# Performance work log

Measured on AMD Instinct MI355X. Metric: run time of the kernel, lower is better.

Reference implementation:

```python
import jax, jax.numpy as jnp
import numpy as np

B, S, E = 2, 2048, 5120
HQ, HKV, HD = 32, 8, 128          # q heads, kv heads, head_dim (hard-coded 128 in source)
DQ, DKV = HQ * HD, HKV * HD       # 4096, 1024
ROPE_THETA = 1.0e9
NEG = -1e30


def setup_inputs() -> dict:
    key = jax.random.key(0)
    k0, k1, k2, k3, k4 = jax.random.split(key, 5)
    x = jax.random.normal(k0, (B, S, E), jnp.float32)
    wq = jax.random.normal(k1, (DQ, E), jnp.float32) * 0.02
    wk = jax.random.normal(k2, (DKV, E), jnp.float32) * 0.02
    wv = jax.random.normal(k3, (DKV, E), jnp.float32) * 0.02
    wo = jax.random.normal(k4, (E, DQ), jnp.float32) * 0.02
    # rotary frequencies: complex freqs_cis[s, HD//2] = exp(i * s * theta^{-2j/HD})
    inv_freq = 1.0 / (ROPE_THETA ** (jnp.arange(0, HD, 2, dtype=jnp.float32) / HD))  # [64]
    ang = jnp.arange(S, dtype=jnp.float32)[:, None] * inv_freq[None, :]              # [S, 64]
    return {
        "x": x,
        "freqs_cos": jnp.cos(ang),
        "freqs_sin": jnp.sin(ang),
        "wq": wq, "wk": wk, "wv": wv, "wo": wo,
    }


def _apply_rope(t, cos, sin):
    # t: [b, s, h, HD//2, 2] viewed as complex pairs; cos/sin: [1, s, 1, HD//2]
    tr, ti = t[..., 0], t[..., 1]
    out = jnp.stack([tr * cos - ti * sin, tr * sin + ti * cos], axis=-1)
    b, s, h = t.shape[0], t.shape[1], t.shape[2]
    return out.reshape(b, s, h, HD)


def reference(x, freqs_cos, freqs_sin, wq, wk, wv, wo):
    b, s, _ = x.shape
    q = (x @ wq.T).reshape(b, s, HQ, HD // 2, 2)
    k = (x @ wk.T).reshape(b, s, HKV, HD // 2, 2)
    v = (x @ wv.T).reshape(b, s, HKV, HD)
    cos = freqs_cos[:s][None, :, None, :]
    sin = freqs_sin[:s][None, :, None, :]
    q = _apply_rope(q, cos, sin)                       # [b, s, HQ, HD]
    k = _apply_rope(k, cos, sin)                       # [b, s, HKV, HD]
    # GQA repeat_kv (repeat_interleave along head dim)
    k = jnp.repeat(k, HQ // HKV, axis=2)               # [b, s, HQ, HD]
    v = jnp.repeat(v, HQ // HKV, axis=2)
    q = q.transpose(0, 2, 1, 3)                        # [b, HQ, s, HD]
    k = k.transpose(0, 2, 1, 3)
    v = v.transpose(0, 2, 1, 3)
    scale = 1.0 / np.sqrt(HD).astype(np.float32)
    scores = jnp.einsum('bhqd,bhkd->bhqk', q, k) * scale
    causal = jnp.tril(jnp.ones((s, s), dtype=bool))
    scores = jnp.where(causal[None, None], scores, NEG)
    attn = jax.nn.softmax(scores, axis=-1)
    out = jnp.einsum('bhqk,bhkd->bhqd', attn, v)       # [b, HQ, s, HD]
    out = out.transpose(0, 2, 1, 3).reshape(b, s, DQ)
    return out @ wo.T                                  # [b, s, E]
```

## Files before the change

### kernel.cpp

```cpp
#include <hip/hip_runtime.h>


typedef unsigned short u16;
typedef __bf16 bf16x8 __attribute__((ext_vector_type(8)));
typedef __bf16 bf16x4 __attribute__((ext_vector_type(4)));
typedef float f32x4 __attribute__((ext_vector_type(4)));

__device__ __forceinline__ u16 f2bf(float f) {
  unsigned u = __builtin_bit_cast(unsigned, f);
  u += 0x7fff + ((u >> 16) & 1);
  return (u16)(u >> 16);
}
__device__ __forceinline__ float bf2f(u16 h) {
  unsigned u = ((unsigned)h) << 16;
  return __builtin_bit_cast(float, u);
}

__device__ __forceinline__ float exp2_hw(float x) {
#if __has_builtin(__builtin_amdgcn_exp2f)
  return __builtin_amdgcn_exp2f(x);
#else
  return __expf(x * 0.6931471805599453f);
#endif
}

__device__ __forceinline__ void gload_lds16(const u16* g, u16* lds) {
  __builtin_amdgcn_global_load_lds(
      (const __attribute__((address_space(1))) void*)g,
      (__attribute__((address_space(3))) void*)lds, 16, 0, 0);
}

__device__ __forceinline__ f32x4 mfma16(bf16x8 a, bf16x8 b, f32x4 c) {
  return __builtin_amdgcn_mfma_f32_16x16x32_bf16(a, b, c, 0, 0, 0);
}

#define VMW(N) asm volatile("s_waitcnt vmcnt(" #N ")" ::: "memory")
#define BAR()  __builtin_amdgcn_s_barrier()

__global__ __launch_bounds__(256) void cvt_kernel(const float4* __restrict__ in,
                                                  uint2* __restrict__ out, int n4) {
  int i = blockIdx.x * blockDim.x + threadIdx.x;
  if (i >= n4) return;
  float4 v = in[i];
  unsigned lo = (unsigned)f2bf(v.x) | ((unsigned)f2bf(v.y) << 16);
  unsigned hi = (unsigned)f2bf(v.z) | ((unsigned)f2bf(v.w) << 16);
  out[i] = make_uint2(lo, hi);
}

__global__ __launch_bounds__(256) void rope_kernel(u16* __restrict__ t,
                                                   const float* __restrict__ fcos,
                                                   const float* __restrict__ fsin,
                                                   int hsh, float scale, int total) {
  int idx = blockIdx.x * blockDim.x + threadIdx.x;
  if (idx >= total) return;
  int j = idx & 63;
  int s = (idx >> (6 + hsh)) & 2047;
  float c = fcos[s * 64 + j], sn = fsin[s * 64 + j];
  unsigned* p = (unsigned*)(t + (size_t)idx * 2);
  unsigned v = *p;
  float tr = bf2f((u16)(v & 0xffffu)), ti = bf2f((u16)(v >> 16));
  float orr = (tr * c - ti * sn) * scale;
  float oi  = (tr * sn + ti * c) * scale;
  *p = (unsigned)f2bf(orr) | ((unsigned)f2bf(oi) << 16);
}

template <int MODE>
__global__ __launch_bounds__(256) void gemm_bt(const u16* __restrict__ A,
                                               const u16* __restrict__ B,
                                               void* __restrict__ Cout,
                                               int M, int N, int K) {
  __shared__ u16 As[8192];
  __shared__ u16 Bs[8192];
  const int tid = threadIdx.x;
  const int lane = tid & 63, wave = tid >> 6;
  const int wm = wave >> 1, wn = wave & 1;
  int gx = gridDim.x, nwg = gx * gridDim.y;
  int lin = blockIdx.y * gx + blockIdx.x;
  if ((nwg & 7) == 0) lin = (lin & 7) * (nwg >> 3) + (lin >> 3);
  const int m0 = (lin / gx) * 128, n0 = (lin % gx) * 128;
  const int lc = lane & 15, lg = lane >> 4;

  f32x4 acc[4][4] = {};
  const int sr = tid >> 3, sc = tid & 7;

  for (int kt = 0; kt < K; kt += 64) {
    __syncthreads();
#pragma unroll
    for (int q = 0; q < 4; ++q) {
      int r = q * 32 + sr;
      int cc = sc ^ (r & 7);
      gload_lds16(A + (size_t)(m0 + r) * K + kt + cc * 8, &As[q * 2048 + tid * 8]);
      gload_lds16(B + (size_t)(n0 + r) * K + kt + cc * 8, &Bs[q * 2048 + tid * 8]);
    }
    __syncthreads();
#pragma unroll
    for (int ks = 0; ks < 2; ++ks) {
      bf16x8 af[4], bfr[4];
#pragma unroll
      for (int m = 0; m < 4; ++m) {
        int r = wm * 64 + m * 16 + lc;
        int gc = ks * 4 + lg;
        af[m] = *(const bf16x8*)&As[r * 64 + ((gc ^ (r & 7)) * 8)];
      }
#pragma unroll
      for (int n = 0; n < 4; ++n) {
        int r = wn * 64 + n * 16 + lc;
        int gc = ks * 4 + lg;
        bfr[n] = *(const bf16x8*)&Bs[r * 64 + ((gc ^ (r & 7)) * 8)];
      }
#pragma unroll
      for (int m = 0; m < 4; ++m)
#pragma unroll
        for (int n = 0; n < 4; ++n)
          acc[m][n] = mfma16(af[m], bfr[n], acc[m][n]);
    }
  }

#pragma unroll
  for (int m = 0; m < 4; ++m) {
#pragma unroll
    for (int n = 0; n < 4; ++n) {
#pragma unroll
      for (int i = 0; i < 4; ++i) {
        int gm = m0 + wm * 64 + m * 16 + lg * 4 + i;
        int gn = n0 + wn * 64 + n * 16 + lc;
        float v = acc[m][n][i];
        if (MODE == 0) {
          ((u16*)Cout)[(size_t)gm * N + gn] = f2bf(v);
        } else if (MODE == 2) {
          size_t addr = ((size_t)((gm >> 11) * 8 + (gn >> 7)) * 128 + (gn & 127)) * 2048 +
                        (gm & 2047);
          ((u16*)Cout)[addr] = f2bf(v);
        } else {
          if (gn < 1024) {
            ((u16*)Cout)[(size_t)gm * 1024 + gn] = f2bf(v);
          } else {
            int gnv = gn - 1024;
            size_t addr = 4194304ull +
                          ((size_t)((gm >> 11) * 8 + (gnv >> 7)) * 128 + (gnv & 127)) * 2048 +
                          (gm & 2047);
            ((u16*)Cout)[addr] = f2bf(v);
          }
        }
      }
    }
  }
}

template <int OUT_F32>
__global__ __launch_bounds__(512, 2) void gemm256(const u16* __restrict__ A,
                                                  const u16* __restrict__ B,
                                                  void* __restrict__ Cout,
                                                  int M, int N, int K) {
  __shared__ u16 lds[2][2][2][8192];
  __shared__ u16 dummy[4096];
  const int tid = threadIdx.x, lane = tid & 63, wave = tid >> 6;
  const int wm = wave >> 2;
  const int wn = wave & 3;
  const int lc = lane & 15, lg = lane >> 4;
  const int bh = wn >> 1;
  const int bs64 = (wn & 1) * 64;
  const int str = tid >> 3, ssc = tid & 7;

  int gx = gridDim.x, nwg = gx * gridDim.y;
  int lin = blockIdx.y * gx + blockIdx.x;
  if ((nwg & 7) == 0) lin = (lin & 7) * (nwg >> 3) + (lin >> 3);
  const int m0 = (lin / gx) * 256, n0 = (lin % gx) * 256;

  auto stageA = [&](int buf, int kcol, int r0, bool real) {
    int r = r0 + str, cc = ssc ^ (r & 7);
    const u16* s = A + (size_t)(m0 + r) * K + kcol + cc * 8;
    u16* d0 = real ? &lds[buf][0][0][r0 * 64] : dummy;
    u16* d1 = real ? &lds[buf][0][1][r0 * 64] : dummy;
    gload_lds16(s, d0 + tid * 8);
    gload_lds16(s + (size_t)128 * K, d1 + tid * 8);
  };
  auto stageB = [&](int buf, int kcol, int half, bool real) {
    int r = str, cc = ssc ^ (r & 7);
    int r2 = 64 + str, cc2 = ssc ^ (r2 & 7);
    const u16* s = B + (size_t)(n0 + half * 128) * K + kcol;
    u16* d0 = real ? &lds[buf][1][half][0] : dummy;
    u16* d1 = real ? &lds[buf][1][half][4096] : dummy;
    gload_lds16(s + (size_t)r * K + cc * 8, d0 + tid * 8);
    gload_lds16(s + (size_t)r2 * K + cc2 * 8, d1 + tid * 8);
  };

  f32x4 acc[8][4] = {};
  bf16x8 af[4][2], bfv[4][2];

  const int nk = K >> 6;
  stageB(0, 0, 0, true);
  stageA(0, 0, 0, true);
  stageB(0, 0, 1, true);
  stageA(0, 0, 64, true);
  stageB(1, 64, 0, true);
  stageA(1, 64, 0, true);
  VMW(6);
  BAR();

  for (int t = 0; t < nk; ++t) {
    const int c = t & 1;
    const int t1 = t + 1, t2 = t + 2;
    const int kc1 = (t1 < nk ? t1 : nk - 1) << 6;
    const int kc2 = (t2 < nk ? t2 : nk - 1) << 6;
    const bool h1 = t1 < nk, h2 = t2 < nk;
    const u16* Ab = &lds[c][0][wm][0];
    const u16* Bb = &lds[c][1][bh][0];

#pragma unroll
    for (int m = 0; m < 4; ++m)
#pragma unroll
      for (int kg = 0; kg < 2; ++kg) {
        int r = m * 16 + lc;
        af[m][kg] = *(const bf16x8*)&Ab[r * 64 + (((kg * 4 + lg) ^ (r & 7)) * 8)];
      }
#pragma unroll
    for (int n = 0; n < 2; ++n)
#pragma unroll
      for (int kg = 0; kg < 2; ++kg) {
        int r = bs64 + n * 16 + lc;
        bfv[n][kg] = *(const bf16x8*)&Bb[r * 64 + (((kg * 4 + lg) ^ (r & 7)) * 8)];
      }
    stageB(t1 & 1, kc1, 1, h1);
    BAR();
    __builtin_amdgcn_s_setprio(1);
#pragma unroll
    for (int m = 0; m < 4; ++m)
#pragma unroll
      for (int n = 0; n < 2; ++n)
#pragma unroll
        for (int kg = 0; kg < 2; ++kg)
          acc[m][n] = mfma16(af[m][kg], bfv[n][kg], acc[m][n]);
    __builtin_amdgcn_s_setprio(0);
    BAR();

#pragma unroll
    for (int n = 2; n < 4; ++n)
#pragma unroll
      for (int kg = 0; kg < 2; ++kg) {
        int r = bs64 + n * 16 + lc;
        bfv[n][kg] = *(const bf16x8*)&Bb[r * 64 + (((kg * 4 + lg) ^ (r & 7)) * 8)];
      }
    stageA(t1 & 1, kc1, 64, h1);
    VMW(6);
    BAR();
    __builtin_amdgcn_s_setprio(1);
#pragma unroll
    for (int m = 0; m < 4; ++m)
#pragma unroll
      for (int n = 2; n < 4; ++n)
#pragma unroll
        for (int kg = 0; kg < 2; ++kg)
          acc[m][n] = mfma16(af[m][kg], bfv[n][kg], acc[m][n]);
    __builtin_amdgcn_s_setprio(0);
    BAR();

#pragma unroll
    for (int m = 0; m < 4; ++m)
#pragma unroll
      for (int kg = 0; kg < 2; ++kg) {
        int r = 64 + m * 16 + lc;
        af[m][kg] = *(const bf16x8*)&Ab[r * 64 + (((kg * 4 + lg) ^ (r & 7)) * 8)];
      }
    stageB(t2 & 1, kc2, 0, h2);
    BAR();
    __builtin_amdgcn_s_setprio(1);
#pragma unroll
    for (int m = 0; m < 4; ++m)
#pragma unroll
      for (int n = 0; n < 2; ++n)
#pragma unroll
        for (int kg = 0; kg < 2; ++kg)
          acc[4 + m][n] = mfma16(af[m][kg], bfv[n][kg], acc[4 + m][n]);
    __builtin_amdgcn_s_setprio(0);
    BAR();

    stageA(t2 & 1, kc2, 0, h2);
    VMW(6);
    BAR();
    __builtin_amdgcn_s_setprio(1);
#pragma unroll
    for (int m = 0; m < 4; ++m)
#pragma unroll
      for (int n = 2; n < 4; ++n)
#pragma unroll
        for (int kg = 0; kg < 2; ++kg)
          acc[4 + m][n] = mfma16(af[m][kg], bfv[n][kg], acc[4 + m][n]);
    __builtin_amdgcn_s_setprio(0);
    BAR();
  }

#pragma unroll
  for (int m = 0; m < 8; ++m) {
#pragma unroll
    for (int n = 0; n < 4; ++n) {
#pragma unroll
      for (int i = 0; i < 4; ++i) {
        int gm = m0 + wm * 128 + m * 16 + lg * 4 + i;
        int gn = n0 + wn * 64 + n * 16 + lc;
        float v = acc[m][n][i];
        if (OUT_F32) ((float*)Cout)[(size_t)gm * N + gn] = v;
        else         ((u16*)Cout)[(size_t)gm * N + gn] = f2bf(v);
      }
    }
  }
}

__global__ __launch_bounds__(512) void attn_kernel(const u16* __restrict__ Q,
                                                   const u16* __restrict__ Kg,
                                                   const u16* __restrict__ VT,
                                                   const float* __restrict__ fcos,
                                                   const float* __restrict__ fsin,
                                                   u16* __restrict__ AO) {
  __shared__ u16 Ks[2][8192];
  __shared__ u16 Vs[2][8192];
  __shared__ u16 P_lds[8][16 * 72];
  const int tid = threadIdx.x, lane = tid & 63, w = tid >> 6;
  const int qt = (int)gridDim.x - 1 - (int)blockIdx.x;
  const int h = blockIdx.y, b = blockIdx.z;
  const int hkv = h >> 2;
  const int q0 = qt * 128;
  const int lc = lane & 15, lg = lane >> 4;

  const float qs = 0.12751743558818574f;
  const int srow = q0 + w * 16 + lc;
  bf16x8 qf[4];
  {
    const size_t qrow = ((size_t)(b * 2048 + srow) * 32 + h) * 128;
#pragma unroll
    for (int ks = 0; ks < 4; ++ks) {
      bf16x8 raw = *(const bf16x8*)&Q[qrow + ks * 32 + lg * 8];
      float4 c4 = *(const float4*)&fcos[srow * 64 + ks * 16 + lg * 4];
      float4 s4 = *(const float4*)&fsin[srow * 64 + ks * 16 + lg * 4];
#pragma unroll
      for (int p = 0; p < 4; ++p) {
        float cc = (&c4.x)[p], ss = (&s4.x)[p];
        float tr = (float)raw[2 * p], ti = (float)raw[2 * p + 1];
        qf[ks][2 * p]     = (__bf16)((tr * cc - ti * ss) * qs);
        qf[ks][2 * p + 1] = (__bf16)((tr * ss + ti * cc) * qs);
      }
    }
  }

  f32x4 o[8] = {};
  f32x4 lsum = {0.f, 0.f, 0.f, 0.f};

  const int nsteps = 2 * qt + 2;
  const size_t kpanel = ((size_t)b * 2048 * 8 + hkv) * 128;
  const size_t vpanel = ((size_t)(b * 8 + hkv) * 128) * 2048;

  auto stage = [&](int buf, int step) {
    const int kv0 = step * 64;
#pragma unroll
    for (int p = 0; p < 2; ++p) {
      int r = p * 32 + (tid >> 4);
      int cc = (tid & 15) ^ (r & 15);
      gload_lds16(Kg + kpanel + (size_t)(kv0 + r) * 1024 + cc * 8,
                  &Ks[buf][p * 4096 + tid * 8]);
    }
#pragma unroll
    for (int p = 0; p < 2; ++p) {
      int r = p * 64 + (tid >> 3);
      int cc = (tid & 7) ^ (r & 7);
      gload_lds16(VT + vpanel + (size_t)r * 2048 + kv0 + cc * 8,
                  &Vs[buf][p * 4096 + tid * 8]);
    }
  };

  stage(0, 0);

  for (int step = 0; step < nsteps; ++step) {
    const int kv0 = step * 64;
    __syncthreads();
    if (step + 1 < nsteps) stage((step + 1) & 1, step + 1);
    const u16* kb = Ks[step & 1];
    const u16* vb = Vs[step & 1];

    f32x4 s[4];
#pragma unroll
    for (int nf = 0; nf < 4; ++nf) s[nf] = f32x4{0.f, 0.f, 0.f, 0.f};
    __builtin_amdgcn_s_setprio(1);
#pragma unroll
    for (int ks = 0; ks < 4; ++ks) {
#pragma unroll
      for (int nf = 0; nf < 4; ++nf) {
        int r = nf * 16 + lc;
        int gc = ks * 4 + lg;
        bf16x8 kf = *(const bf16x8*)&kb[r * 128 + ((gc ^ (r & 15)) * 8)];
        s[nf] = mfma16(kf, qf[ks], s[nf]);
      }
    }
    __builtin_amdgcn_s_setprio(0);

    if (step >= 2 * qt) {
      int q = srow;
#pragma unroll
      for (int nf = 0; nf < 4; ++nf) {
#pragma unroll
        for (int i = 0; i < 4; ++i) {
          int kv = kv0 + nf * 16 + lg * 4 + i;
          if (kv > q) s[nf][i] = -1e30f;
        }
      }
    }

#pragma unroll
    for (int nf = 0; nf < 4; ++nf) {
#pragma unroll
      for (int i = 0; i < 4; ++i) s[nf][i] = exp2_hw(s[nf][i]);
      lsum += s[nf];
      bf16x4 pw = {(__bf16)s[nf][0], (__bf16)s[nf][1], (__bf16)s[nf][2], (__bf16)s[nf][3]};
      *(bf16x4*)&P_lds[w][lc * 72 + nf * 16 + lg * 4] = pw;
    }
    asm volatile("s_waitcnt lgkmcnt(0)" ::: "memory");
    __builtin_amdgcn_sched_barrier(0);

    bf16x8 pa[2];
#pragma unroll
    for (int ksv = 0; ksv < 2; ++ksv)
      pa[ksv] = *(const bf16x8*)&P_lds[w][lc * 72 + ksv * 32 + lg * 8];

    __builtin_amdgcn_s_setprio(1);
#pragma unroll
    for (int nfd = 0; nfd < 8; ++nfd) {
#pragma unroll
      for (int ksv = 0; ksv < 2; ++ksv) {
        int r = nfd * 16 + lc;
        int gc = ksv * 4 + lg;
        bf16x8 vf = *(const bf16x8*)&vb[r * 64 + ((gc ^ (r & 7)) * 8)];
        o[nfd] = mfma16(pa[ksv], vf, o[nfd]);
      }
    }
    __builtin_amdgcn_s_setprio(0);
  }

  float t = lsum[0] + lsum[1] + lsum[2] + lsum[3];
  t += __shfl_xor(t, 16, 64);
  t += __shfl_xor(t, 32, 64);
  float linv[4];
#pragma unroll
  for (int i = 0; i < 4; ++i) linv[i] = 1.0f / __shfl(t, lg * 4 + i, 64);

#pragma unroll
  for (int nfd = 0; nfd < 8; ++nfd)
#pragma unroll
    for (int i = 0; i < 4; ++i) {
      int row = q0 + w * 16 + lg * 4 + i;
      AO[((size_t)(b * 2048 + row) * 32 + h) * 128 + nfd * 16 + lc] =
          f2bf(o[nfd][i] * linv[i]);
    }
}

extern "C" void kernel_launch(void* const* d_in, const int* in_sizes, int n_in,
                              void* d_out, int out_size, void* d_ws, size_t ws_size,
                              hipStream_t stream) {
  const float* x    = (const float*)d_in[0];
  const float* fcos = (const float*)d_in[1];
  const float* fsin = (const float*)d_in[2];
  const float* wq   = (const float*)d_in[3];
  const float* wk   = (const float*)d_in[4];
  const float* wv   = (const float*)d_in[5];
  const float* wo   = (const float*)d_in[6];
  float* out = (float*)d_out;

  char* ws = (char*)d_ws;
  u16* xb  = (u16*)(ws + 0);
  u16* wqb = (u16*)(ws + 41943040ull);
  u16* wkb = (u16*)(ws + 83886080ull);
  u16* wvb = (u16*)(ws + 94371840ull);
  u16* Qb  = (u16*)(ws + 104857600ull);
  u16* Kb  = (u16*)(ws + 138412032ull);
  u16* VTb = (u16*)(ws + 146800640ull);
  u16* AOb = xb;
  u16* wob = wqb;

  auto cvt = [&](const float* src, u16* dst, int nelem) {
    int n4 = nelem / 4;
    cvt_kernel<<<dim3((n4 + 255) / 256), dim3(256), 0, stream>>>((const float4*)src,
                                                                 (uint2*)dst, n4);
  };
  cvt(x, xb, 2 * 2048 * 5120);
  cvt(wq, wqb, 4096 * 5120);
  cvt(wk, wkb, 1024 * 5120);
  cvt(wv, wvb, 1024 * 5120);

  dim3 blk(256);
  gemm256<0><<<dim3(16, 16), dim3(512), 0, stream>>>(xb, wqb, Qb, 4096, 4096, 5120);
  gemm_bt<3><<<dim3(16, 32), blk, 0, stream>>>(xb, wkb, Kb, 4096, 2048, 5120);

  cvt(wo, wob, 5120 * 4096);

  rope_kernel<<<dim3(2097152 / 256), blk, 0, stream>>>(Kb, fcos, fsin, 3, 1.0f, 2097152);

  attn_kernel<<<dim3(16, 32, 2), dim3(512), 0, stream>>>(Qb, Kb, VTb, fcos, fsin, AOb);

  gemm256<1><<<dim3(20, 16), dim3(512), 0, stream>>>(AOb, wob, out, 4096, 5120, 4096);
}
```

Before: 749.1 us.

## Software-pipeline attention loop: overlap next-step QK with current softmax and PV

Restructures the attention main loop into a two-stage software pipeline: the QK^T MFMAs for step t+1 are issued before the softmax and PV work for step t. K staging is split from V staging so K can be loaded two steps ahead. K is triple-buffered in LDS to make room for this, and the loop is unrolled by two with alternating score registers. The aim is to hide exp and LDS latency behind matrix work. The cost is more LDS use, more live registers and an extra barrier per step.

```diff
diff --git a/kernel.cpp b/kernel.cpp
--- a/kernel.cpp
+++ b/kernel.cpp
@@ -312,7 +312,7 @@
                                                    const float* __restrict__ fcos,
                                                    const float* __restrict__ fsin,
                                                    u16* __restrict__ AO) {
-  __shared__ u16 Ks[2][8192];
+  __shared__ u16 Ks[3][8192];
   __shared__ u16 Vs[2][8192];
   __shared__ u16 P_lds[8][16 * 72];
   const int tid = threadIdx.x, lane = tid & 63, w = tid >> 6;
@@ -349,7 +349,7 @@
   const size_t kpanel = ((size_t)b * 2048 * 8 + hkv) * 128;
   const size_t vpanel = ((size_t)(b * 8 + hkv) * 128) * 2048;
 
-  auto stage = [&](int buf, int step) {
+  auto stageK = [&](int buf, int step) {
     const int kv0 = step * 64;
 #pragma unroll
     for (int p = 0; p < 2; ++p) {
@@ -358,6 +358,9 @@
       gload_lds16(Kg + kpanel + (size_t)(kv0 + r) * 1024 + cc * 8,
                   &Ks[buf][p * 4096 + tid * 8]);
     }
+  };
+  auto stageV = [&](int buf, int step) {
+    const int kv0 = step * 64;
 #pragma unroll
     for (int p = 0; p < 2; ++p) {
       int r = p * 64 + (tid >> 3);
@@ -367,16 +370,8 @@
     }
   };
 
-  stage(0, 0);
-
-  for (int step = 0; step < nsteps; ++step) {
-    const int kv0 = step * 64;
-    __syncthreads();
-    if (step + 1 < nsteps) stage((step + 1) & 1, step + 1);
-    const u16* kb = Ks[step & 1];
-    const u16* vb = Vs[step & 1];
-
-    f32x4 s[4];
+  auto qk = [&](f32x4* s, int step) {
+    const u16* kb = Ks[step % 3];
 #pragma unroll
     for (int nf = 0; nf < 4; ++nf) s[nf] = f32x4{0.f, 0.f, 0.f, 0.f};
     __builtin_amdgcn_s_setprio(1);
@@ -391,19 +386,18 @@
       }
     }
     __builtin_amdgcn_s_setprio(0);
-
+  };
+
+  auto softpv = [&](f32x4* s, int step) {
     if (step >= 2 * qt) {
-      int q = srow;
-#pragma unroll
-      for (int nf = 0; nf < 4; ++nf) {
+#pragma unroll
+      for (int nf = 0; nf < 4; ++nf)
 #pragma unroll
         for (int i = 0; i < 4; ++i) {
-          int kv = kv0 + nf * 16 + lg * 4 + i;
-          if (kv > q) s[nf][i] = -1e30f;
+          int kv = step * 64 + nf * 16 + lg * 4 + i;
+          if (kv > srow) s[nf][i] = -1e30f;
         }
-      }
-    }
-
+    }
 #pragma unroll
     for (int nf = 0; nf < 4; ++nf) {
 #pragma unroll
@@ -414,12 +408,11 @@
     }
     asm volatile("s_waitcnt lgkmcnt(0)" ::: "memory");
     __builtin_amdgcn_sched_barrier(0);
-
     bf16x8 pa[2];
 #pragma unroll
     for (int ksv = 0; ksv < 2; ++ksv)
       pa[ksv] = *(const bf16x8*)&P_lds[w][lc * 72 + ksv * 32 + lg * 8];
-
+    const u16* vb = Vs[step & 1];
     __builtin_amdgcn_s_setprio(1);
 #pragma unroll
     for (int nfd = 0; nfd < 8; ++nfd) {
@@ -432,6 +425,25 @@
       }
     }
     __builtin_amdgcn_s_setprio(0);
+  };
+
+  f32x4 sA[4], sB[4];
+  stageK(0, 0); stageV(0, 0);
+  __syncthreads();
+  stageK(1, 1);
+  qk(sA, 0);
+
+  for (int t = 0; t < nsteps; t += 2) {
+    __syncthreads();
+    if (t + 2 < nsteps) stageK((t + 2) % 3, t + 2);
+    if (t + 1 < nsteps) stageV((t + 1) & 1, t + 1);
+    if (t + 1 < nsteps) qk(sB, t + 1);
+    softpv(sA, t);
+    __syncthreads();
+    if (t + 3 < nsteps) stageK((t + 3) % 3, t + 3);
+    if (t + 2 < nsteps) stageV((t + 2) & 1, t + 2);
+    if (t + 2 < nsteps) qk(sA, t + 2);
+    softpv(sB, t + 1);
   }
 
   float t = lsum[0] + lsum[1] + lsum[2] + lsum[3];
```

Result: no change. 756.5 us (+1.0%).

## Remap GEMM workgroups to XCD-local 2D tile blocks and fuse input conversions

Applied to the files above, without the earlier changes.

Replaces the linear XCD-interleave workgroup remap in both GEMM kernels with a 2D decomposition. Each of the 8 XCDs now owns a contiguous rectangular block of output tiles, so A and B panels are reused within that XCD's L2. Also merges the four separate fp32-to-bf16 conversion launches into one grid-stride kernel to cut launch overhead. The remap falls back to a plain row-major order when grid dimensions do not divide evenly. The fused converter adds per-element branching to select the source array.

```diff
diff --git a/kernel.cpp b/kernel.cpp
--- a/kernel.cpp
+++ b/kernel.cpp
@@ -36,6 +36,29 @@
 
 #define VMW(N) asm volatile("s_waitcnt vmcnt(" #N ")" ::: "memory")
 #define BAR()  __builtin_amdgcn_s_barrier()
+
+__global__ __launch_bounds__(256) void cvt4_kernel(const float4* __restrict__ s0,
+                                                   const float4* __restrict__ s1,
+                                                   const float4* __restrict__ s2,
+                                                   const float4* __restrict__ s3,
+                                                   uint2* __restrict__ d0,
+                                                   uint2* __restrict__ d1,
+                                                   uint2* __restrict__ d2,
+                                                   uint2* __restrict__ d3,
+                                                   int n0, int n1, int n2, int n3) {
+  int total = n0 + n1 + n2 + n3;
+  for (int i = blockIdx.x * blockDim.x + threadIdx.x; i < total;
+       i += gridDim.x * blockDim.x) {
+    const float4* s; uint2* d; int j = i;
+    if (j < n0) { s = s0; d = d0; }
+    else if ((j -= n0) < n1) { s = s1; d = d1; }
+    else if ((j -= n1) < n2) { s = s2; d = d2; }
+    else { j -= n2; s = s3; d = d3; }
+    float4 v = s[j];
+    d[j] = make_uint2((unsigned)f2bf(v.x) | ((unsigned)f2bf(v.y) << 16),
+                      (unsigned)f2bf(v.z) | ((unsigned)f2bf(v.w) << 16));
+  }
+}
 
 __global__ __launch_bounds__(256) void cvt_kernel(const float4* __restrict__ in,
                                                   uint2* __restrict__ out, int n4) {
@@ -74,10 +97,18 @@
   const int tid = threadIdx.x;
   const int lane = tid & 63, wave = tid >> 6;
   const int wm = wave >> 1, wn = wave & 1;
-  int gx = gridDim.x, nwg = gx * gridDim.y;
-  int lin = blockIdx.y * gx + blockIdx.x;
-  if ((nwg & 7) == 0) lin = (lin & 7) * (nwg >> 3) + (lin >> 3);
-  const int m0 = (lin / gx) * 128, n0 = (lin % gx) * 128;
+  int gx = gridDim.x, gy = gridDim.y, nwg = gx * gy;
+  int orig = blockIdx.y * gx + blockIdx.x;
+  int mb, nb;
+  if ((gx & 1) == 0 && (gy & 3) == 0 && (nwg & 7) == 0) {
+    int x = orig & 7, idx = orig >> 3;
+    int hy = gy >> 2, qx = gx >> 1;
+    mb = (x >> 1) * hy + (idx % hy);
+    nb = (x & 1) * qx + (idx / hy);
+  } else {
+    mb = orig / gx; nb = orig % gx;
+  }
+  const int m0 = mb * 128, n0 = nb * 128;
   const int lc = lane & 15, lg = lane >> 4;
 
   f32x4 acc[4][4] = {};
@@ -162,10 +193,18 @@
   const int bs64 = (wn & 1) * 64;
   const int str = tid >> 3, ssc = tid & 7;
 
-  int gx = gridDim.x, nwg = gx * gridDim.y;
-  int lin = blockIdx.y * gx + blockIdx.x;
-  if ((nwg & 7) == 0) lin = (lin & 7) * (nwg >> 3) + (lin >> 3);
-  const int m0 = (lin / gx) * 256, n0 = (lin % gx) * 256;
+  int gx = gridDim.x, gy = gridDim.y;
+  int orig = blockIdx.y * gx + blockIdx.x;
+  int mb, nb;
+  if ((gx & 3) == 0 && (gy & 1) == 0) {
+    int x = orig & 7, idx = orig >> 3;
+    int hy = gy >> 1, qx = gx >> 2;
+    mb = (x >> 2) * hy + (idx % hy);
+    nb = (x & 3) * qx + (idx / hy);
+  } else {
+    mb = orig / gx; nb = orig % gx;
+  }
+  const int m0 = mb * 256, n0 = nb * 256;
 
   auto stageA = [&](int buf, int kcol, int r0, bool real) {
     int r = r0 + str, cc = ssc ^ (r & 7);
@@ -474,21 +513,17 @@
   u16* AOb = xb;
   u16* wob = wqb;
 
-  auto cvt = [&](const float* src, u16* dst, int nelem) {
-    int n4 = nelem / 4;
-    cvt_kernel<<<dim3((n4 + 255) / 256), dim3(256), 0, stream>>>((const float4*)src,
-                                                                 (uint2*)dst, n4);
-  };
-  cvt(x, xb, 2 * 2048 * 5120);
-  cvt(wq, wqb, 4096 * 5120);
-  cvt(wk, wkb, 1024 * 5120);
-  cvt(wv, wvb, 1024 * 5120);
+  cvt4_kernel<<<dim3(2048), dim3(256), 0, stream>>>(
+      (const float4*)x, (const float4*)wq, (const float4*)wk, (const float4*)wv,
+      (uint2*)xb, (uint2*)wqb, (uint2*)wkb, (uint2*)wvb,
+      2 * 2048 * 5120 / 4, 4096 * 5120 / 4, 1024 * 5120 / 4, 1024 * 5120 / 4);
 
   dim3 blk(256);
   gemm256<0><<<dim3(16, 16), dim3(512), 0, stream>>>(xb, wqb, Qb, 4096, 4096, 5120);
   gemm_bt<3><<<dim3(16, 32), blk, 0, stream>>>(xb, wkb, Kb, 4096, 2048, 5120);
 
-  cvt(wo, wob, 5120 * 4096);
+  cvt_kernel<<<dim3(5242880 / 256), blk, 0, stream>>>((const float4*)wo, (uint2*)wob,
+                                                      5242880);
 
   rope_kernel<<<dim3(2097152 / 256), blk, 0, stream>>>(Kb, fcos, fsin, 3, 1.0f, 2097152);
 
```

New measurement: 731.6 us. 2.3% less time.
